# Optimization experiments

Measured on AMD Instinct MI355X. Metric: run time of the kernel, lower is better.

The kernel has to match this reference:

```python
import jax, jax.numpy as jnp
import numpy as np

N_EMBD = 1024
N_HEAD = 16

def setup_inputs() -> dict:
    key = jax.random.key(0)
    ks = jax.random.split(key, 6)
    C = N_EMBD
    s = 1.0 / np.sqrt(C)
    x = jax.random.normal(ks[0], (4, 2048, C), dtype=jnp.float32)
    Wk = jax.random.normal(ks[1], (C, C), dtype=jnp.float32) * s
    Wq = jax.random.normal(ks[2], (C, C), dtype=jnp.float32) * s
    Wv = jax.random.normal(ks[3], (C, C), dtype=jnp.float32) * s
    Wp = jax.random.normal(ks[4], (C, C), dtype=jnp.float32) * s
    bp = jax.random.normal(ks[5], (C,), dtype=jnp.float32) * 0.01
    return {"x": x, "Wq": Wq, "Wk": Wk, "Wv": Wv, "Wp": Wp, "bp": bp}

def reference(x, Wq, Wk, Wv, Wp, bp):
    B, T, C = x.shape
    H = N_HEAD
    d = C // H
    # projections (bias=False)
    q = (x @ Wq).reshape(B, T, H, d).transpose(0, 2, 1, 3)  # [B,H,T,d]
    k = (x @ Wk).reshape(B, T, H, d).transpose(0, 2, 1, 3)
    v = (x @ Wv).reshape(B, T, H, d).transpose(0, 2, 1, 3)
    att = jnp.einsum('bhqd,bhkd->bhqk', q, k) * (1.0 / np.sqrt(d))
    causal = jnp.tril(jnp.ones((T, T), dtype=bool))
    att = jnp.where(causal[None, None], att, jnp.float32(-jnp.inf))
    att = jax.nn.softmax(att, axis=-1)
    y = jnp.einsum('bhqk,bhkd->bhqd', att, v)  # [B,H,T,d]
    y = y.transpose(0, 2, 1, 3).reshape(B, T, C)
    return y @ Wp + bp
```

## Files before the change

kernel.cpp:

```cpp
#include <hip/hip_runtime.h>
#include <hip/hip_bf16.h>

#define N_EMBD 1024
#define N_HEADS 16
#define HD 64
#define TSEQ 2048
#define BATCH 4
#define M_TOT (BATCH*TSEQ)

typedef short s16x8 __attribute__((ext_vector_type(8)));
typedef float f32x4 __attribute__((ext_vector_type(4)));

__device__ __forceinline__ void glds16(const void* g, void* l) {
  __builtin_amdgcn_global_load_lds((const __attribute__((address_space(1))) void*)g,
                                   (__attribute__((address_space(3))) void*)l, 16, 0, 0);
}

__device__ __forceinline__ float exp_scaled(float s) {
  float r;
  asm("v_exp_f32 %0, %1\n\ts_nop 0" : "=v"(r) : "v"(s * 0.18033688011112042f));
  return r;
}

__device__ __forceinline__ unsigned cvtpk(float lo, float hi) {
  unsigned r;
  asm("v_cvt_pk_bf16_f32 %0, %1, %2" : "=v"(r) : "v"(lo), "v"(hi));
  return r;
}

__global__ __launch_bounds__(256) void xcast_kernel(const float* __restrict__ x,
                                                    __hip_bfloat16* __restrict__ xb) {
  int i = blockIdx.x * 256 + threadIdx.x;
  float4 f = ((const float4*)x)[i];
  __hip_bfloat162 p0, p1;
  p0.x = __float2bfloat16(f.x); p0.y = __float2bfloat16(f.y);
  p1.x = __float2bfloat16(f.z); p1.y = __float2bfloat16(f.w);
  ((__hip_bfloat162*)xb)[2*i]   = p0;
  ((__hip_bfloat162*)xb)[2*i+1] = p1;
}

__global__ void wcast_kernel(const float* __restrict__ Wq, const float* __restrict__ Wk,
                             const float* __restrict__ Wv, const float* __restrict__ Wp,
                             __hip_bfloat16* __restrict__ wqkvt, __hip_bfloat16* __restrict__ wpt) {
  __shared__ float tile[32][33];
  int z = blockIdx.z;
  const float* in = (z==0)?Wq:(z==1)?Wk:(z==2)?Wv:Wp;
  __hip_bfloat16* out = (z<3) ? (wqkvt + (size_t)z*N_EMBD*N_EMBD) : wpt;
  int tx = threadIdx.x, ty = threadIdx.y;
  int x  = blockIdx.x*32 + tx;
  int y0 = blockIdx.y*32;
  #pragma unroll
  for (int j=0;j<4;++j) tile[ty + j*8][tx] = in[(size_t)(y0+ty+j*8)*N_EMBD + x];
  __syncthreads();
  int xo  = y0 + tx;
  int yo0 = blockIdx.x*32;
  #pragma unroll
  for (int j=0;j<4;++j)
    out[(size_t)(yo0+ty+j*8)*N_EMBD + xo] = __float2bfloat16(tile[tx][ty+j*8]);
}

__global__ __launch_bounds__(256) void gemm_kernel(
    const __hip_bfloat16* __restrict__ A,
    const __hip_bfloat16* __restrict__ Bt,
    __hip_bfloat16* __restrict__ Qb, __hip_bfloat16* __restrict__ Kb,
    __hip_bfloat16* __restrict__ Vt,
    float* __restrict__ out, const float* __restrict__ bias, int mode) {
  __shared__ __align__(16) char smem[32768];
  __hip_bfloat16* Alin = (__hip_bfloat16*)smem;
  __hip_bfloat16* Blin = (__hip_bfloat16*)(smem + 16384);
  int tid = threadIdx.x;
  int m0 = blockIdx.y*128, n0 = blockIdx.x*128;
  int w = tid>>6, lane = tid&63, l16 = lane&15, quad = lane>>4;
  int wr = w>>1, wc = w&1;
  int xg = l16 & 7;
  int off0 = ((quad    ) ^ xg)*8;
  int off1 = ((quad + 4) ^ xg)*8;
  f32x4 acc[4][4];
  #pragma unroll
  for (int mi=0;mi<4;++mi)
    #pragma unroll
    for (int ni=0;ni<4;++ni) acc[mi][ni] = (f32x4){0.f,0.f,0.f,0.f};

  for (int k0=0; k0<N_EMBD; k0+=64) {
    __syncthreads();
    #pragma unroll
    for (int rd=0; rd<4; ++rd) {
      int slot = rd*256 + tid;
      int row  = slot>>3;
      int gc8  = ((tid&7) ^ (row&7))*8;
      glds16(A  + (size_t)(m0+row)*N_EMBD + k0 + gc8, Alin + slot*8);
      glds16(Bt + (size_t)(n0+row)*N_EMBD + k0 + gc8, Blin + slot*8);
    }
    __syncthreads();
    #pragma unroll
    for (int c=0;c<2;++c) {
      int off = c ? off1 : off0;
      s16x8 af[4], bfr[4];
      #pragma unroll
      for (int mi=0;mi<4;++mi)
        af[mi] = *(const s16x8*)(Alin + (wr*64+mi*16+l16)*64 + off);
      #pragma unroll
      for (int ni=0;ni<4;++ni)
        bfr[ni] = *(const s16x8*)(Blin + (wc*64+ni*16+l16)*64 + off);
      #pragma unroll
      for (int mi=0;mi<4;++mi)
        #pragma unroll
        for (int ni=0;ni<4;++ni)
          acc[mi][ni] = __builtin_amdgcn_mfma_f32_16x16x32_bf16(af[mi], bfr[ni], acc[mi][ni],0,0,0);
    }
  }

  if (mode == 0) {
    int which = n0 >> 10;
    int bb = m0 >> 11, t0 = m0 & 2047;
    if (which < 2) {
      __hip_bfloat16* outp = (which==0)?Qb:Kb;
      #pragma unroll
      for (int mi=0;mi<4;++mi) {
        #pragma unroll
        for (int ni=0;ni<4;++ni) {
          int ncol = (n0 & 1023) + wc*64 + ni*16 + l16;
          int hh = ncol>>6, dd = ncol&63;
          #pragma unroll
          for (int r=0;r<4;++r) {
            int t = t0 + wr*64 + mi*16 + quad*4 + r;
            outp[((size_t)(bb*N_HEADS + hh)*TSEQ + t)*HD + dd] = __float2bfloat16(acc[mi][ni][r]);
          }
        }
      }
    } else {
      int hh0 = (n0 & 1023) >> 6;
      __hip_bfloat16 (*Ts)[136] = (__hip_bfloat16(*)[136])smem;
      #pragma unroll
      for (int p=0;p<2;++p) {
        __syncthreads();
        if (wc == p) {
          #pragma unroll
          for (int mi=0;mi<4;++mi)
            #pragma unroll
            for (int ni=0;ni<4;++ni) {
              int dd = ni*16 + l16;
              #pragma unroll
              for (int r=0;r<4;++r)
                Ts[dd][wr*64 + mi*16 + quad*4 + r] = __float2bfloat16(acc[mi][ni][r]);
            }
        }
        __syncthreads();
        int dd = tid>>2, tc = (tid&3)*32;
        __hip_bfloat16* dst = Vt + ((size_t)(bb*N_HEADS + hh0 + p)*HD + dd)*TSEQ + t0 + tc;
        #pragma unroll
        for (int c4=0;c4<4;++c4)
          *(uint4*)(dst + c4*8) = *(const uint4*)&Ts[dd][tc + c4*8];
      }
    }
  } else {
    #pragma unroll
    for (int mi=0;mi<4;++mi) {
      #pragma unroll
      for (int ni=0;ni<4;++ni) {
        int col = n0 + wc*64 + ni*16 + l16;
        float bs = bias[col];
        #pragma unroll
        for (int r=0;r<4;++r) {
          int m = m0 + wr*64 + mi*16 + quad*4 + r;
          out[(size_t)m*N_EMBD + col] = acc[mi][ni][r] + bs;
        }
      }
    }
  }
}

__global__ __launch_bounds__(256) void attn_kernel(
    const __hip_bfloat16* __restrict__ Qb, const __hip_bfloat16* __restrict__ Kb,
    const __hip_bfloat16* __restrict__ Vt, __hip_bfloat16* __restrict__ Yb) {
  __shared__ __align__(16) __hip_bfloat16 Ks[2][64][64];
  __shared__ __align__(16) __hip_bfloat16 Vs[2][64][64];
  int tid = threadIdx.x;
  int b = blockIdx.z, h = blockIdx.y;
  int qb = (b & 1) ? (TSEQ/128 - 1 - blockIdx.x) : blockIdx.x;
  int q0 = qb*128;
  size_t bhT  = (size_t)(b*N_HEADS + h)*TSEQ;
  size_t bhHD = (size_t)(b*N_HEADS + h)*HD;
  int lane = tid&63, w = tid>>6, l16 = lane&15, quad = lane>>4;
  int wq = w*32;
  int xg = l16 & 7;
  int off0 = ((quad    ) ^ xg)*8;
  int off1 = ((quad + 4) ^ xg)*8;
  int q21 = quad>>1, q1 = (quad&1)*4;
  int vo[2][2];
  vo[0][0] = ((0 + q21) ^ xg)*8 + q1;
  vo[0][1] = ((2 + q21) ^ xg)*8 + q1;
  vo[1][0] = ((4 + q21) ^ xg)*8 + q1;
  vo[1][1] = ((6 + q21) ^ xg)*8 + q1;

  int slot0 = tid,        row0 = slot0>>3, gcA = ((tid&7) ^ (row0&7))*8;
  int slot1 = 256 + tid,  row1 = slot1>>3, gcB = ((tid&7) ^ (row1&7))*8;

  s16x8 qf[2][2];
  #pragma unroll
  for (int mi=0;mi<2;++mi) {
    const __hip_bfloat16* qrow = Qb + (bhT + q0 + wq + mi*16 + l16)*HD;
    qf[mi][0] = *(const s16x8*)(qrow + quad*8);
    qf[mi][1] = *(const s16x8*)(qrow + 32 + quad*8);
  }

  f32x4 z4 = {0.f,0.f,0.f,0.f};
  f32x4 oacc[4][2];
  #pragma unroll
  for (int nd=0;nd<4;++nd) { oacc[nd][0]=z4; oacc[nd][1]=z4; }
  float lsum[2] = {0.f, 0.f};

  int ntiles = 2*qb + 2;

  {
    glds16(Kb + (bhT + 0 + row0)*HD + gcA,    &Ks[0][0][0] + slot0*8);
    glds16(Vt + (bhHD + row0)*TSEQ + 0 + gcA, &Vs[0][0][0] + slot0*8);
    glds16(Kb + (bhT + 0 + row1)*HD + gcB,    &Ks[0][0][0] + slot1*8);
    glds16(Vt + (bhHD + row1)*TSEQ + 0 + gcB, &Vs[0][0][0] + slot1*8);
  }

  for (int t=0; t<ntiles; ++t) {
    int cur = t&1;
    int k0 = t*64;
    if (t+1 < ntiles) {
      int kn = k0 + 64;
      glds16(Kb + (bhT + kn + row0)*HD + gcA,     &Ks[cur^1][0][0] + slot0*8);
      glds16(Vt + (bhHD + row0)*TSEQ + kn + gcA,  &Vs[cur^1][0][0] + slot0*8);
      glds16(Kb + (bhT + kn + row1)*HD + gcB,     &Ks[cur^1][0][0] + slot1*8);
      glds16(Vt + (bhHD + row1)*TSEQ + kn + gcB,  &Vs[cur^1][0][0] + slot1*8);
      asm volatile("s_waitcnt vmcnt(4)" ::: "memory");
    } else {
      asm volatile("s_waitcnt vmcnt(0)" ::: "memory");
    }
    __builtin_amdgcn_s_barrier();
    __builtin_amdgcn_sched_barrier(0);

    const __hip_bfloat16* Kc = &Ks[cur][0][0];
    const __hip_bfloat16* Vc = &Vs[cur][0][0];

    f32x4 sacc[4][2];
    #pragma unroll
    for (int ni=0; ni<4; ++ni) {
      s16x8 kb0 = *(const s16x8*)(Kc + (ni*16+l16)*64 + off0);
      s16x8 kb1 = *(const s16x8*)(Kc + (ni*16+l16)*64 + off1);
      #pragma unroll
      for (int mi=0; mi<2; ++mi) {
        f32x4 s = z4;
        s = __builtin_amdgcn_mfma_f32_16x16x32_bf16(kb0, qf[mi][0], s,0,0,0);
        s = __builtin_amdgcn_mfma_f32_16x16x32_bf16(kb1, qf[mi][1], s,0,0,0);
        sacc[ni][mi] = s;
      }
    }

    unsigned pkw[2][4][2];
    if (q0 + wq >= k0 + 63) {
      #pragma unroll
      for (int ni=0; ni<4; ++ni) {
        #pragma unroll
        for (int mi=0; mi<2; ++mi) {
          float e0 = exp_scaled(sacc[ni][mi][0]);
          float e1 = exp_scaled(sacc[ni][mi][1]);
          float e2 = exp_scaled(sacc[ni][mi][2]);
          float e3 = exp_scaled(sacc[ni][mi][3]);
          lsum[mi] += (e0+e1)+(e2+e3);
          pkw[mi][ni][0] = cvtpk(e0, e1);
          pkw[mi][ni][1] = cvtpk(e2, e3);
        }
      }
    } else {
      #pragma unroll
      for (int ni=0; ni<4; ++ni) {
        int kbase = k0 + ni*16 + quad*4;
        #pragma unroll
        for (int mi=0; mi<2; ++mi) {
          int qrow = q0 + wq + mi*16 + l16;
          float e0 = (qrow >= kbase    ) ? exp_scaled(sacc[ni][mi][0]) : 0.f;
          float e1 = (qrow >= kbase + 1) ? exp_scaled(sacc[ni][mi][1]) : 0.f;
          float e2 = (qrow >= kbase + 2) ? exp_scaled(sacc[ni][mi][2]) : 0.f;
          float e3 = (qrow >= kbase + 3) ? exp_scaled(sacc[ni][mi][3]) : 0.f;
          lsum[mi] += (e0+e1)+(e2+e3);
          pkw[mi][ni][0] = cvtpk(e0, e1);
          pkw[mi][ni][1] = cvtpk(e2, e3);
        }
      }
    }

    union U8 { s16x8 v; unsigned u[4]; uint2 u2[2]; };
    #pragma unroll
    for (int c=0; c<2; ++c) {
      U8 pf0, pf1;
      pf0.u[0] = pkw[0][2*c][0];   pf0.u[1] = pkw[0][2*c][1];
      pf0.u[2] = pkw[0][2*c+1][0]; pf0.u[3] = pkw[0][2*c+1][1];
      pf1.u[0] = pkw[1][2*c][0];   pf1.u[1] = pkw[1][2*c][1];
      pf1.u[2] = pkw[1][2*c+1][0]; pf1.u[3] = pkw[1][2*c+1][1];
      #pragma unroll
      for (int nd=0; nd<4; ++nd) {
        const __hip_bfloat16* vrow = Vc + (nd*16 + l16)*64;
        U8 vf;
        vf.u2[0] = *(const uint2*)(vrow + vo[c][0]);
        vf.u2[1] = *(const uint2*)(vrow + vo[c][1]);
        oacc[nd][0] = __builtin_amdgcn_mfma_f32_16x16x32_bf16(vf.v, pf0.v, oacc[nd][0],0,0,0);
        oacc[nd][1] = __builtin_amdgcn_mfma_f32_16x16x32_bf16(vf.v, pf1.v, oacc[nd][1],0,0,0);
      }
    }

    asm volatile("s_waitcnt lgkmcnt(0)" ::: "memory");
    __builtin_amdgcn_s_barrier();
    __builtin_amdgcn_sched_barrier(0);
  }

  #pragma unroll
  for (int mi=0; mi<2; ++mi) {
    lsum[mi] += __shfl_xor(lsum[mi], 16);
    lsum[mi] += __shfl_xor(lsum[mi], 32);
  }

  #pragma unroll
  for (int mi=0; mi<2; ++mi) {
    float inv = 1.f / lsum[mi];
    int tq = q0 + wq + mi*16 + l16;
    __hip_bfloat16* yr = Yb + ((size_t)(b*TSEQ + tq))*N_EMBD + h*HD + quad*4;
    #pragma unroll
    for (int nd=0; nd<4; ++nd) {
      uint2 o;
      o.x = cvtpk(oacc[nd][mi][0]*inv, oacc[nd][mi][1]*inv);
      o.y = cvtpk(oacc[nd][mi][2]*inv, oacc[nd][mi][3]*inv);
      *(uint2*)(yr + nd*16) = o;
    }
  }
}

extern "C" void kernel_launch(void* const* d_in, const int* in_sizes, int n_in,
                              void* d_out, int out_size, void* d_ws, size_t ws_size,
                              hipStream_t stream) {
  const float* x  = (const float*)d_in[0];
  const float* Wq = (const float*)d_in[1];
  const float* Wk = (const float*)d_in[2];
  const float* Wv = (const float*)d_in[3];
  const float* Wp = (const float*)d_in[4];
  const float* bp = (const float*)d_in[5];

  char* w = (char*)d_ws;
  __hip_bfloat16* xb    = (__hip_bfloat16*)w;  w += (size_t)M_TOT*N_EMBD*2;
  __hip_bfloat16* wqkvt = (__hip_bfloat16*)w;  w += (size_t)3*N_EMBD*N_EMBD*2;
  __hip_bfloat16* wpt   = (__hip_bfloat16*)w;  w += (size_t)N_EMBD*N_EMBD*2;
  __hip_bfloat16* Qb    = (__hip_bfloat16*)w;  w += (size_t)M_TOT*N_EMBD*2;
  __hip_bfloat16* Kb    = (__hip_bfloat16*)w;  w += (size_t)M_TOT*N_EMBD*2;
  __hip_bfloat16* Vt    = (__hip_bfloat16*)w;  w += (size_t)M_TOT*N_EMBD*2;
  __hip_bfloat16* Yb    = (__hip_bfloat16*)w;

  xcast_kernel<<<dim3(M_TOT*N_EMBD/1024), dim3(256), 0, stream>>>(x, xb);
  wcast_kernel<<<dim3(32,32,4), dim3(32,8), 0, stream>>>(Wq,Wk,Wv,Wp,wqkvt,wpt);
  gemm_kernel<<<dim3(24,64), dim3(256), 0, stream>>>(xb, wqkvt, Qb,Kb,Vt, nullptr, nullptr, 0);
  attn_kernel<<<dim3(TSEQ/128,N_HEADS,BATCH), dim3(256), 0, stream>>>(Qb,Kb,Vt,Yb);
  gemm_kernel<<<dim3(8,64), dim3(256), 0, stream>>>(Yb, wpt, nullptr,nullptr,nullptr,
                                                    (float*)d_out, bp, 1);
}
```

Before: 270.8 us.

## Pre-permute transposed V in global memory so attention reads 16-byte V fragments

The QKV projection epilogue now writes the transposed V tensor with a key permutation inside each 64-wide block. The permutation matches the order in which the attention kernel consumes P fragments. The attention PV loop can then load each V operand with one 16-byte LDS read at the same swizzled offsets used for K, replacing two 8-byte reads, and the per-thread vo offset table is dropped. The cost is a scatter of 8-byte stores in the epilogue instead of 16-byte stores, and correctness now depends on the permutation exactly matching the P packing.

Result: no change. 268.9 us (-0.7%).

```diff
diff --git a/kernel.cpp b/kernel.cpp
--- a/kernel.cpp
+++ b/kernel.cpp
@@ -147,10 +147,14 @@
         }
         __syncthreads();
         int dd = tid>>2, tc = (tid&3)*32;
-        __hip_bfloat16* dst = Vt + ((size_t)(bb*N_HEADS + hh0 + p)*HD + dd)*TSEQ + t0 + tc;
-        #pragma unroll
-        for (int c4=0;c4<4;++c4)
-          *(uint4*)(dst + c4*8) = *(const uint4*)&Ts[dd][tc + c4*8];
+        __hip_bfloat16* dst = Vt + ((size_t)(bb*N_HEADS + hh0 + p)*HD + dd)*TSEQ + t0;
+        #pragma unroll
+        for (int pb=0; pb<8; ++pb) {
+          int q  = tc + pb*4;
+          int pp = q & 63;
+          int key = (q & 64) | (pp & 32) | ((pp & 4) << 2) | ((pp & 24) >> 1);
+          *(uint2*)(dst + q) = *(const uint2*)&Ts[dd][key];
+        }
       }
     }
   } else {
@@ -186,12 +190,6 @@
   int xg = l16 & 7;
   int off0 = ((quad    ) ^ xg)*8;
   int off1 = ((quad + 4) ^ xg)*8;
-  int q21 = quad>>1, q1 = (quad&1)*4;
-  int vo[2][2];
-  vo[0][0] = ((0 + q21) ^ xg)*8 + q1;
-  vo[0][1] = ((2 + q21) ^ xg)*8 + q1;
-  vo[1][0] = ((4 + q21) ^ xg)*8 + q1;
-  vo[1][1] = ((6 + q21) ^ xg)*8 + q1;
 
   int slot0 = tid,        row0 = slot0>>3, gcA = ((tid&7) ^ (row0&7))*8;
   int slot1 = 256 + tid,  row1 = slot1>>3, gcB = ((tid&7) ^ (row1&7))*8;
@@ -285,23 +283,26 @@
       }
     }
 
-    union U8 { s16x8 v; unsigned u[4]; uint2 u2[2]; };
-    #pragma unroll
-    for (int c=0; c<2; ++c) {
-      U8 pf0, pf1;
-      pf0.u[0] = pkw[0][2*c][0];   pf0.u[1] = pkw[0][2*c][1];
-      pf0.u[2] = pkw[0][2*c+1][0]; pf0.u[3] = pkw[0][2*c+1][1];
-      pf1.u[0] = pkw[1][2*c][0];   pf1.u[1] = pkw[1][2*c][1];
-      pf1.u[2] = pkw[1][2*c+1][0]; pf1.u[3] = pkw[1][2*c+1][1];
-      #pragma unroll
-      for (int nd=0; nd<4; ++nd) {
-        const __hip_bfloat16* vrow = Vc + (nd*16 + l16)*64;
-        U8 vf;
-        vf.u2[0] = *(const uint2*)(vrow + vo[c][0]);
-        vf.u2[1] = *(const uint2*)(vrow + vo[c][1]);
-        oacc[nd][0] = __builtin_amdgcn_mfma_f32_16x16x32_bf16(vf.v, pf0.v, oacc[nd][0],0,0,0);
-        oacc[nd][1] = __builtin_amdgcn_mfma_f32_16x16x32_bf16(vf.v, pf1.v, oacc[nd][1],0,0,0);
-      }
+    union U8 { s16x8 v; unsigned u[4]; };
+    U8 pf[2][2];
+    #pragma unroll
+    for (int c=0; c<2; ++c)
+      #pragma unroll
+      for (int mi=0; mi<2; ++mi) {
+        pf[c][mi].u[0] = pkw[mi][2*c  ][0];
+        pf[c][mi].u[1] = pkw[mi][2*c  ][1];
+        pf[c][mi].u[2] = pkw[mi][2*c+1][0];
+        pf[c][mi].u[3] = pkw[mi][2*c+1][1];
+      }
+    #pragma unroll
+    for (int nd=0; nd<4; ++nd) {
+      const __hip_bfloat16* vrow = Vc + (nd*16 + l16)*64;
+      s16x8 vb0 = *(const s16x8*)(vrow + off0);
+      s16x8 vb1 = *(const s16x8*)(vrow + off1);
+      oacc[nd][0] = __builtin_amdgcn_mfma_f32_16x16x32_bf16(vb0, pf[0][0].v, oacc[nd][0],0,0,0);
+      oacc[nd][1] = __builtin_amdgcn_mfma_f32_16x16x32_bf16(vb0, pf[0][1].v, oacc[nd][1],0,0,0);
+      oacc[nd][0] = __builtin_amdgcn_mfma_f32_16x16x32_bf16(vb1, pf[1][0].v, oacc[nd][0],0,0,0);
+      oacc[nd][1] = __builtin_amdgcn_mfma_f32_16x16x32_bf16(vb1, pf[1][1].v, oacc[nd][1],0,0,0);
     }
 
     asm volatile("s_waitcnt lgkmcnt(0)" ::: "memory");
```
